# Performance work log

Hardware: AMD Instinct MI355X
Metric: run time of the kernel (lower is better)

The kernel has to match this reference:

```python
import jax, jax.numpy as jnp
import numpy as np

EPS = 1e-12  # torch F.normalize eps

def _l2n(x, axis):
    n = jnp.linalg.norm(x, axis=axis, keepdims=True)
    return x / jnp.maximum(n, EPS)

def setup_inputs() -> dict:
    key = jax.random.key(0)
    ks = jax.random.split(key, 11)
    B, N, D = 8, 4096, 512
    s = 1.0 / np.sqrt(D)
    return {
        'a': jax.random.normal(ks[0], (B, N, D), jnp.float32),
        'b': jax.random.normal(ks[1], (B, N, D), jnp.float32),
        'Wq': jax.random.normal(ks[2], (D, D), jnp.float32) * s,
        'bq': jax.random.normal(ks[3], (D,), jnp.float32) * s,
        'Wk': jax.random.normal(ks[4], (D, D), jnp.float32) * s,
        'bk': jax.random.normal(ks[5], (D,), jnp.float32) * s,
        'w_g': jax.random.normal(ks[6], (D, 1), jnp.float32),
        'Wp': jax.random.normal(ks[7], (D, D), jnp.float32) * s,
        'bp': jax.random.normal(ks[8], (D,), jnp.float32) * s,
        'Wf': jax.random.normal(ks[9], (D, D), jnp.float32) * s,
        'bf': jax.random.normal(ks[10], (D,), jnp.float32) * s,
    }

def reference(a, b, Wq, bq, Wk, bk, w_g, Wp, bp, Wf, bf):
    D = a.shape[-1]
    scale = D ** (-0.5)
    query = _l2n(jnp.einsum('bnd,ed->bne', a, Wq) + bq, axis=-1)   # [B,N,D]
    key = _l2n(jnp.einsum('bnd,ed->bne', b, Wk) + bk, axis=-1)     # [B,N,D]
    A = (query @ w_g) * scale                                      # [B,N,1]
    A = _l2n(A, axis=1)                                            # normalize over seq
    G = jnp.sum(A * query, axis=1)                                 # [B,D] learned pooling
    gk = G[:, None, :] * key                                       # broadcast [B,N,D]
    out = jnp.einsum('bnd,ed->bne', gk, Wp) + bp + query           # residual
    out = jnp.einsum('bnd,ed->bne', out, Wf) + bf
    return out
```

## Files before the change

### kernel.cpp

```cpp
#include <hip/hip_runtime.h>
#include <stdint.h>

#define DD 512
#define MTOT 32768

typedef float f32x4 __attribute__((ext_vector_type(4)));
typedef __bf16 bf16x8 __attribute__((ext_vector_type(8)));

static __device__ __forceinline__ unsigned short f2bf(float f) {
  union { float f; unsigned int u; } c; c.f = f;
  unsigned int r = c.u + 0x7fffu + ((c.u >> 16) & 1u);
  return (unsigned short)(r >> 16);
}
static __device__ __forceinline__ float bf2f(unsigned short h) {
  union { unsigned int u; float f; } c; c.u = ((unsigned int)h) << 16;
  return c.f;
}

union FragU { uint4 u; bf16x8 b; };

static __device__ __forceinline__ void load_lds16(const void* g, void* l) {
  __builtin_amdgcn_global_load_lds(
      (const __attribute__((address_space(1))) void*)g,
      (__attribute__((address_space(3))) void*)l, 16, 0, 0);
}

__global__ __launch_bounds__(256) void cvt_k(const float* __restrict__ src,
                                             unsigned short* __restrict__ dst) {
  int i = (blockIdx.x * 256 + threadIdx.x) * 4;
  float4 f = *(const float4*)(src + i);
  ushort4 h;
  h.x = f2bf(f.x); h.y = f2bf(f.y); h.z = f2bf(f.z); h.w = f2bf(f.w);
  *(ushort4*)(dst + i) = h;
}

__global__ __launch_bounds__(256) void cvt3w_k(const float* __restrict__ W0,
    const float* __restrict__ W1, const float* __restrict__ W2,
    unsigned short* __restrict__ D0, unsigned short* __restrict__ D1,
    unsigned short* __restrict__ D2) {
  int slab = blockIdx.x >> 8;
  int off = ((blockIdx.x & 255) * 256 + threadIdx.x) * 4;
  const float* s = slab == 0 ? W0 : slab == 1 ? W1 : W2;
  unsigned short* d = slab == 0 ? D0 : slab == 1 ? D1 : D2;
  float4 f = *(const float4*)(s + off);
  ushort4 h;
  h.x = f2bf(f.x); h.y = f2bf(f.y); h.z = f2bf(f.z); h.w = f2bf(f.w);
  *(ushort4*)(d + off) = h;
}

__global__ __launch_bounds__(256) void scalew_k(const float* __restrict__ Wp,
    const float* __restrict__ G, unsigned short* __restrict__ out) {
  int i = (blockIdx.x * 256 + threadIdx.x) * 4;
  int b = i >> 18;
  int rem = i & 262143;
  int d = rem & 511;
  float4 w = *(const float4*)(Wp + rem);
  float4 g = *(const float4*)(G + b * DD + d);
  ushort4 h;
  h.x = f2bf(w.x * g.x); h.y = f2bf(w.y * g.y);
  h.z = f2bf(w.z * g.z); h.w = f2bf(w.w * g.w);
  *(ushort4*)(out + i) = h;
}

template<int BBATCH, int EMODE>
__global__ __launch_bounds__(256) void gemm_k(
    const unsigned short* __restrict__ X,
    const unsigned short* __restrict__ Wb,
    const float* __restrict__ bias,
    const unsigned short* __restrict__ Qadd,
    void* __restrict__ Cv) {
  __shared__ unsigned short As[128 * 64];
  __shared__ unsigned short Bs[128 * 64];
  const int tid = threadIdx.x;
  const int lane = tid & 63, wave = tid >> 6;
  const int row0 = blockIdx.x * 128, col0 = blockIdx.y * 128;
  const unsigned short* W = Wb + (BBATCH ? (size_t)(row0 >> 12) * 262144 : 0);

  const int sr = lane >> 3;
  const int scol = ((lane & 7) ^ sr) * 8;
  const unsigned short* Ag = X + (size_t)(row0 + wave * 32 + sr) * DD + scol;
  const unsigned short* Bg = W + (size_t)(col0 + wave * 32 + sr) * DD + scol;
  const int ldsb = wave * 32 * 64;

  const int fr = lane & 15, quad = lane >> 4;
  const int wr = (wave >> 1) * 64, wc = (wave & 1) * 64;
  const int sw0 = ((quad ^ (fr & 7)) * 8);
  const int sw1 = (((quad + 4) ^ (fr & 7)) * 8);

  f32x4 acc[4][4] = {};

  for (int k0 = 0; k0 < DD; k0 += 64) {
#pragma unroll
    for (int q = 0; q < 4; q++) {
      load_lds16(Ag + (size_t)q * 8 * DD + k0, As + ldsb + q * 8 * 64);
      load_lds16(Bg + (size_t)q * 8 * DD + k0, Bs + ldsb + q * 8 * 64);
    }
    __syncthreads();
#pragma unroll
    for (int kk = 0; kk < 2; kk++) {
      const int sw = kk ? sw1 : sw0;
      bf16x8 af[4], bfr[4];
#pragma unroll
      for (int i = 0; i < 4; i++) {
        FragU u; u.u = *(const uint4*)&As[(wr + i * 16 + fr) * 64 + sw];
        af[i] = u.b;
      }
#pragma unroll
      for (int j = 0; j < 4; j++) {
        FragU u; u.u = *(const uint4*)&Bs[(wc + j * 16 + fr) * 64 + sw];
        bfr[j] = u.b;
      }
#pragma unroll
      for (int i = 0; i < 4; i++)
#pragma unroll
        for (int j = 0; j < 4; j++)
          acc[i][j] = __builtin_amdgcn_mfma_f32_16x16x32_bf16(af[i], bfr[j], acc[i][j], 0, 0, 0);
    }
    __syncthreads();
  }
#pragma unroll
  for (int j = 0; j < 4; j++) {
    int gc = col0 + wc + j * 16 + fr;
    float bv = bias[gc];
#pragma unroll
    for (int i = 0; i < 4; i++) {
      int gr0 = row0 + wr + i * 16 + quad * 4;
#pragma unroll
      for (int r = 0; r < 4; r++) {
        size_t idx = (size_t)(gr0 + r) * DD + gc;
        float v = acc[i][j][r] + bv;
        if (EMODE == 1) v += bf2f(Qadd[idx]);
        if (EMODE <= 1) ((unsigned short*)Cv)[idx] = f2bf(v);
        else            ((float*)Cv)[idx] = v;
      }
    }
  }
}

__global__ __launch_bounds__(256) void norm_k(unsigned short* __restrict__ Q,
    unsigned short* __restrict__ K, const float* __restrict__ wg,
    float* __restrict__ Araw) {
  const int lane = threadIdx.x & 63, wave = threadIdx.x >> 6;
  const size_t row = (size_t)blockIdx.x * 4 + wave;
  unsigned short* p = (blockIdx.y == 0 ? Q : K) + row * DD + lane * 8;
  uint4 u = *(uint4*)p;
  unsigned short* hp = (unsigned short*)&u;
  float v[8];
  float ss = 0.f;
#pragma unroll
  for (int t = 0; t < 8; t++) { v[t] = bf2f(hp[t]); ss += v[t] * v[t]; }
#pragma unroll
  for (int m = 1; m < 64; m <<= 1) ss += __shfl_xor(ss, m, 64);
  float inv = 1.0f / fmaxf(sqrtf(ss), 1e-12f);
#pragma unroll
  for (int t = 0; t < 8; t++) { v[t] *= inv; hp[t] = f2bf(v[t]); }
  *(uint4*)p = u;
  if (blockIdx.y == 0) {
    const float4* wp = (const float4*)(wg + lane * 8);
    float4 w0 = wp[0], w1 = wp[1];
    float dot = v[0] * w0.x + v[1] * w0.y + v[2] * w0.z + v[3] * w0.w +
                v[4] * w1.x + v[5] * w1.y + v[6] * w1.z + v[7] * w1.w;
#pragma unroll
    for (int m = 1; m < 64; m <<= 1) dot += __shfl_xor(dot, m, 64);
    if (lane == 0) Araw[row] = dot;
  }
}

__global__ __launch_bounds__(512) void reduce_s_k(const float* __restrict__ Araw,
    float* __restrict__ sinv, float* __restrict__ G) {
  const int b = blockIdx.x, t = threadIdx.x;
  G[b * DD + t] = 0.f;
  float ss = 0.f;
  for (int i = t; i < 4096; i += 512) { float v = Araw[b * 4096 + i]; ss += v * v; }
#pragma unroll
  for (int m = 1; m < 64; m <<= 1) ss += __shfl_xor(ss, m, 64);
  __shared__ float sred[8];
  if ((t & 63) == 0) sred[t >> 6] = ss;
  __syncthreads();
  if (t == 0) {
    float tot = 0.f;
    for (int i = 0; i < 8; i++) tot += sred[i];
    sinv[b] = 1.0f / fmaxf(sqrtf(tot), 1e-12f);
  }
}

__global__ __launch_bounds__(256) void pool_k(const float* __restrict__ Araw,
    const float* __restrict__ sinv, const unsigned short* __restrict__ Q,
    float* __restrict__ G) {
  const int b = blockIdx.x >> 5;
  const int chunk = blockIdx.x & 31;
  const int rbase = b * 4096 + chunk * 128;
  const float si = sinv[b];
  const int t = threadIdx.x;
  float a0 = 0.f, a1 = 0.f;
  for (int r = 0; r < 128; r++) {
    float w = Araw[rbase + r] * si;
    const unsigned short* qr = Q + (size_t)(rbase + r) * DD;
    a0 += w * bf2f(qr[t]);
    a1 += w * bf2f(qr[t + 256]);
  }
  atomicAdd(&G[b * DD + t], a0);
  atomicAdd(&G[b * DD + t + 256], a1);
}

extern "C" void kernel_launch(void* const* d_in, const int* in_sizes, int n_in,
                              void* d_out, int out_size, void* d_ws, size_t ws_size,
                              hipStream_t stream) {
  const float* a   = (const float*)d_in[0];
  const float* b   = (const float*)d_in[1];
  const float* Wq  = (const float*)d_in[2];
  const float* bq  = (const float*)d_in[3];
  const float* Wk  = (const float*)d_in[4];
  const float* bk  = (const float*)d_in[5];
  const float* wg  = (const float*)d_in[6];
  const float* Wp  = (const float*)d_in[7];
  const float* bp  = (const float*)d_in[8];
  const float* Wf  = (const float*)d_in[9];
  const float* bfb = (const float*)d_in[10];

  const size_t WELEM = 262144;
  const size_t MD = (size_t)MTOT * DD;

  unsigned short* ABb = (unsigned short*)d_ws;
  unsigned short* Qb  = ABb + MD;
  unsigned short* Kb  = Qb + MD;
  unsigned short* Wqb = Kb + MD;
  unsigned short* Wkb = Wqb + WELEM;
  unsigned short* Wfb = Wkb + WELEM;
  unsigned short* Wps = Wfb + WELEM;
  float* Araw = (float*)(Wps + 8 * WELEM);
  float* sinv = Araw + MTOT;
  float* G    = sinv + 64;

  cvt_k<<<dim3(16384), dim3(256), 0, stream>>>(a, ABb);
  cvt3w_k<<<dim3(768), dim3(256), 0, stream>>>(Wq, Wk, Wf, Wqb, Wkb, Wfb);
  gemm_k<0, 0><<<dim3(256, 4), dim3(256), 0, stream>>>(ABb, Wqb, bq, nullptr, Qb);
  cvt_k<<<dim3(16384), dim3(256), 0, stream>>>(b, ABb);
  gemm_k<0, 0><<<dim3(256, 4), dim3(256), 0, stream>>>(ABb, Wkb, bk, nullptr, Kb);
  norm_k<<<dim3(MTOT / 4, 2), dim3(256), 0, stream>>>(Qb, Kb, wg, Araw);
  reduce_s_k<<<dim3(8), dim3(512), 0, stream>>>(Araw, sinv, G);
  pool_k<<<dim3(256), dim3(256), 0, stream>>>(Araw, sinv, Qb, G);
  scalew_k<<<dim3(2048), dim3(256), 0, stream>>>(Wp, G, Wps);
  gemm_k<1, 1><<<dim3(256, 4), dim3(256), 0, stream>>>(Kb, Wps, bp, Qb, ABb);
  gemm_k<0, 2><<<dim3(256, 4), dim3(256), 0, stream>>>(ABb, Wfb, bfb, nullptr, d_out);
}
```

Baseline: 329.2 us.

## Fuse fp32->bf16 input conversion and row-norm statistics into GEMM epilogues

The Q and K projection GEMMs now read fp32 activations directly and convert them to bf16 while staging into LDS, which removes the separate conversion passes. Their epilogues accumulate per-row sums of squares and the w_g dot product through atomics. The separate normalization pass is dropped: Q and K stay unnormalized, and the per-row inverse norms are applied inside the later residual GEMM epilogue and in the pooling weights. The trade-offs are synchronous register-path loads for A in place of async LDS loads, extra atomics, and an unnormalized bf16 Q/K that changes rounding.

```diff
diff --git a/kernel.cpp b/kernel.cpp
--- a/kernel.cpp
+++ b/kernel.cpp
@@ -25,20 +25,16 @@
       (__attribute__((address_space(3))) void*)l, 16, 0, 0);
 }
 
-__global__ __launch_bounds__(256) void cvt_k(const float* __restrict__ src,
-                                             unsigned short* __restrict__ dst) {
-  int i = (blockIdx.x * 256 + threadIdx.x) * 4;
-  float4 f = *(const float4*)(src + i);
-  ushort4 h;
-  h.x = f2bf(f.x); h.y = f2bf(f.y); h.z = f2bf(f.z); h.w = f2bf(f.w);
-  *(ushort4*)(dst + i) = h;
-}
-
 __global__ __launch_bounds__(256) void cvt3w_k(const float* __restrict__ W0,
     const float* __restrict__ W1, const float* __restrict__ W2,
     unsigned short* __restrict__ D0, unsigned short* __restrict__ D1,
-    unsigned short* __restrict__ D2) {
+    unsigned short* __restrict__ D2, float* __restrict__ stats) {
   int slab = blockIdx.x >> 8;
+  if (slab == 3) {
+    int i = ((blockIdx.x - 768) * 256 + threadIdx.x) * 4;
+    *(float4*)(stats + i) = make_float4(0.f, 0.f, 0.f, 0.f);
+    return;
+  }
   int off = ((blockIdx.x & 255) * 256 + threadIdx.x) * 4;
   const float* s = slab == 0 ? W0 : slab == 1 ? W1 : W2;
   unsigned short* d = slab == 0 ? D0 : slab == 1 ? D1 : D2;
@@ -62,12 +58,17 @@
   *(ushort4*)(out + i) = h;
 }
 
-template<int BBATCH, int EMODE>
+template<int XFP32, int BBATCH, int EMODE>
 __global__ __launch_bounds__(256) void gemm_k(
-    const unsigned short* __restrict__ X,
+    const void* __restrict__ Xv,
     const unsigned short* __restrict__ Wb,
     const float* __restrict__ bias,
     const unsigned short* __restrict__ Qadd,
+    const float* __restrict__ wg,
+    float* __restrict__ ssq,
+    float* __restrict__ Pdot,
+    const float* __restrict__ qinv,
+    const float* __restrict__ kinv,
     void* __restrict__ Cv) {
   __shared__ unsigned short As[128 * 64];
   __shared__ unsigned short Bs[128 * 64];
@@ -77,10 +78,13 @@
   const unsigned short* W = Wb + (BBATCH ? (size_t)(row0 >> 12) * 262144 : 0);
 
   const int sr = lane >> 3;
-  const int scol = ((lane & 7) ^ sr) * 8;
-  const unsigned short* Ag = X + (size_t)(row0 + wave * 32 + sr) * DD + scol;
-  const unsigned short* Bg = W + (size_t)(col0 + wave * 32 + sr) * DD + scol;
+  const int c8 = lane & 7;
+  const unsigned short* Ag =
+      (const unsigned short*)Xv + (size_t)(row0 + wave * 32 + sr) * DD + (c8 ^ sr) * 8;
+  const unsigned short* Bg = W + (size_t)(col0 + wave * 32 + sr) * DD + (c8 ^ sr) * 8;
+  const float* Agf = (const float*)Xv + (size_t)(row0 + wave * 32 + sr) * DD + c8 * 8;
   const int ldsb = wave * 32 * 64;
+  const int awr = ldsb + sr * 64 + (c8 ^ sr) * 8;
 
   const int fr = lane & 15, quad = lane >> 4;
   const int wr = (wave >> 1) * 64, wc = (wave & 1) * 64;
@@ -92,7 +96,19 @@
   for (int k0 = 0; k0 < DD; k0 += 64) {
 #pragma unroll
     for (int q = 0; q < 4; q++) {
-      load_lds16(Ag + (size_t)q * 8 * DD + k0, As + ldsb + q * 8 * 64);
+      if (XFP32) {
+        const float* s = Agf + (size_t)q * 8 * DD + k0;
+        f32x4 f0 = *(const f32x4*)s;
+        f32x4 f1 = *(const f32x4*)(s + 4);
+        union { uint4 u; unsigned short h[8]; } pk;
+        pk.h[0] = f2bf(f0.x); pk.h[1] = f2bf(f0.y);
+        pk.h[2] = f2bf(f0.z); pk.h[3] = f2bf(f0.w);
+        pk.h[4] = f2bf(f1.x); pk.h[5] = f2bf(f1.y);
+        pk.h[6] = f2bf(f1.z); pk.h[7] = f2bf(f1.w);
+        *(uint4*)&As[awr + q * 8 * 64] = pk.u;
+      } else {
+        load_lds16(Ag + (size_t)q * 8 * DD + k0, As + ldsb + q * 8 * 64);
+      }
       load_lds16(Bg + (size_t)q * 8 * DD + k0, Bs + ldsb + q * 8 * 64);
     }
     __syncthreads();
@@ -118,60 +134,67 @@
     }
     __syncthreads();
   }
-#pragma unroll
-  for (int j = 0; j < 4; j++) {
-    int gc = col0 + wc + j * 16 + fr;
-    float bv = bias[gc];
-#pragma unroll
-    for (int i = 0; i < 4; i++) {
-      int gr0 = row0 + wr + i * 16 + quad * 4;
-#pragma unroll
-      for (int r = 0; r < 4; r++) {
-        size_t idx = (size_t)(gr0 + r) * DD + gc;
-        float v = acc[i][j][r] + bv;
-        if (EMODE == 1) v += bf2f(Qadd[idx]);
-        if (EMODE <= 1) ((unsigned short*)Cv)[idx] = f2bf(v);
+
+  const int colbase = col0 + wc + fr;
+  float bv4[4];
+#pragma unroll
+  for (int j = 0; j < 4; j++) bv4[j] = bias[colbase + j * 16];
+  float wg4[4];
+  if (EMODE == 1) {
+#pragma unroll
+    for (int j = 0; j < 4; j++) wg4[j] = wg[colbase + j * 16];
+  }
+#pragma unroll
+  for (int i = 0; i < 4; i++) {
+#pragma unroll
+    for (int r = 0; r < 4; r++) {
+      const int row = row0 + wr + i * 16 + quad * 4 + r;
+      float ki = 1.f, qi = 1.f;
+      if (EMODE == 3) { ki = kinv[row]; qi = qinv[row]; }
+      float ssum = 0.f, dsum = 0.f;
+#pragma unroll
+      for (int j = 0; j < 4; j++) {
+        size_t idx = (size_t)row * DD + colbase + j * 16;
+        float v;
+        if (EMODE == 3) v = acc[i][j][r] * ki + bv4[j] + qi * bf2f(Qadd[idx]);
+        else            v = acc[i][j][r] + bv4[j];
+        if (EMODE != 4) ((unsigned short*)Cv)[idx] = f2bf(v);
         else            ((float*)Cv)[idx] = v;
+        if (EMODE == 1 || EMODE == 2) ssum += v * v;
+        if (EMODE == 1) dsum += v * wg4[j];
+      }
+      if (EMODE == 1 || EMODE == 2) {
+#pragma unroll
+        for (int m = 1; m < 16; m <<= 1) ssum += __shfl_xor(ssum, m, 64);
+        if (EMODE == 1) {
+#pragma unroll
+          for (int m = 1; m < 16; m <<= 1) dsum += __shfl_xor(dsum, m, 64);
+        }
+        if (fr == 0) {
+          atomicAdd(&ssq[row], ssum);
+          if (EMODE == 1) atomicAdd(&Pdot[row], dsum);
+        }
       }
     }
   }
 }
 
-__global__ __launch_bounds__(256) void norm_k(unsigned short* __restrict__ Q,
-    unsigned short* __restrict__ K, const float* __restrict__ wg,
-    float* __restrict__ Araw) {
-  const int lane = threadIdx.x & 63, wave = threadIdx.x >> 6;
-  const size_t row = (size_t)blockIdx.x * 4 + wave;
-  unsigned short* p = (blockIdx.y == 0 ? Q : K) + row * DD + lane * 8;
-  uint4 u = *(uint4*)p;
-  unsigned short* hp = (unsigned short*)&u;
-  float v[8];
-  float ss = 0.f;
-#pragma unroll
-  for (int t = 0; t < 8; t++) { v[t] = bf2f(hp[t]); ss += v[t] * v[t]; }
-#pragma unroll
-  for (int m = 1; m < 64; m <<= 1) ss += __shfl_xor(ss, m, 64);
-  float inv = 1.0f / fmaxf(sqrtf(ss), 1e-12f);
-#pragma unroll
-  for (int t = 0; t < 8; t++) { v[t] *= inv; hp[t] = f2bf(v[t]); }
-  *(uint4*)p = u;
-  if (blockIdx.y == 0) {
-    const float4* wp = (const float4*)(wg + lane * 8);
-    float4 w0 = wp[0], w1 = wp[1];
-    float dot = v[0] * w0.x + v[1] * w0.y + v[2] * w0.z + v[3] * w0.w +
-                v[4] * w1.x + v[5] * w1.y + v[6] * w1.z + v[7] * w1.w;
-#pragma unroll
-    for (int m = 1; m < 64; m <<= 1) dot += __shfl_xor(dot, m, 64);
-    if (lane == 0) Araw[row] = dot;
-  }
-}
-
-__global__ __launch_bounds__(512) void reduce_s_k(const float* __restrict__ Araw,
-    float* __restrict__ sinv, float* __restrict__ G) {
+__global__ __launch_bounds__(512) void finstat_k(const float* __restrict__ ssqQ,
+    const float* __restrict__ ssqK, const float* __restrict__ P,
+    float* __restrict__ qinv, float* __restrict__ kinv,
+    float* __restrict__ Araw2, float* __restrict__ sinv, float* __restrict__ G) {
   const int b = blockIdx.x, t = threadIdx.x;
   G[b * DD + t] = 0.f;
   float ss = 0.f;
-  for (int i = t; i < 4096; i += 512) { float v = Araw[b * 4096 + i]; ss += v * v; }
+  for (int i = t; i < 4096; i += 512) {
+    int n = b * 4096 + i;
+    float qi = 1.0f / fmaxf(sqrtf(ssqQ[n]), 1e-12f);
+    float ki = 1.0f / fmaxf(sqrtf(ssqK[n]), 1e-12f);
+    qinv[n] = qi; kinv[n] = ki;
+    float A = P[n] * qi;
+    Araw2[n] = A * qi;
+    ss += A * A;
+  }
 #pragma unroll
   for (int m = 1; m < 64; m <<= 1) ss += __shfl_xor(ss, m, 64);
   __shared__ float sred[8];
@@ -184,7 +207,7 @@
   }
 }
 
-__global__ __launch_bounds__(256) void pool_k(const float* __restrict__ Araw,
+__global__ __launch_bounds__(256) void pool_k(const float* __restrict__ Araw2,
     const float* __restrict__ sinv, const unsigned short* __restrict__ Q,
     float* __restrict__ G) {
   const int b = blockIdx.x >> 5;
@@ -194,7 +217,7 @@
   const int t = threadIdx.x;
   float a0 = 0.f, a1 = 0.f;
   for (int r = 0; r < 128; r++) {
-    float w = Araw[rbase + r] * si;
+    float w = Araw2[rbase + r] * si;
     const unsigned short* qr = Q + (size_t)(rbase + r) * DD;
     a0 += w * bf2f(qr[t]);
     a1 += w * bf2f(qr[t + 256]);
@@ -221,26 +244,33 @@
   const size_t WELEM = 262144;
   const size_t MD = (size_t)MTOT * DD;
 
-  unsigned short* ABb = (unsigned short*)d_ws;
-  unsigned short* Qb  = ABb + MD;
+  unsigned short* O1b = (unsigned short*)d_ws;
+  unsigned short* Qb  = O1b + MD;
   unsigned short* Kb  = Qb + MD;
   unsigned short* Wqb = Kb + MD;
   unsigned short* Wkb = Wqb + WELEM;
   unsigned short* Wfb = Wkb + WELEM;
   unsigned short* Wps = Wfb + WELEM;
-  float* Araw = (float*)(Wps + 8 * WELEM);
-  float* sinv = Araw + MTOT;
-  float* G    = sinv + 64;
-
-  cvt_k<<<dim3(16384), dim3(256), 0, stream>>>(a, ABb);
-  cvt3w_k<<<dim3(768), dim3(256), 0, stream>>>(Wq, Wk, Wf, Wqb, Wkb, Wfb);
-  gemm_k<0, 0><<<dim3(256, 4), dim3(256), 0, stream>>>(ABb, Wqb, bq, nullptr, Qb);
-  cvt_k<<<dim3(16384), dim3(256), 0, stream>>>(b, ABb);
-  gemm_k<0, 0><<<dim3(256, 4), dim3(256), 0, stream>>>(ABb, Wkb, bk, nullptr, Kb);
-  norm_k<<<dim3(MTOT / 4, 2), dim3(256), 0, stream>>>(Qb, Kb, wg, Araw);
-  reduce_s_k<<<dim3(8), dim3(512), 0, stream>>>(Araw, sinv, G);
-  pool_k<<<dim3(256), dim3(256), 0, stream>>>(Araw, sinv, Qb, G);
+  float* stats = (float*)(Wps + 8 * WELEM);
+  float* ssqQ  = stats;
+  float* ssqK  = stats + MTOT;
+  float* Pd    = stats + 2 * MTOT;
+  float* qinv  = stats + 3 * MTOT;
+  float* kinv  = stats + 4 * MTOT;
+  float* Araw2 = stats + 5 * MTOT;
+  float* sinv  = stats + 6 * MTOT;
+  float* G     = sinv + 64;
+
+  cvt3w_k<<<dim3(864), dim3(256), 0, stream>>>(Wq, Wk, Wf, Wqb, Wkb, Wfb, stats);
+  gemm_k<1, 0, 1><<<dim3(256, 4), dim3(256), 0, stream>>>(
+      a, Wqb, bq, nullptr, wg, ssqQ, Pd, nullptr, nullptr, Qb);
+  gemm_k<1, 0, 2><<<dim3(256, 4), dim3(256), 0, stream>>>(
+      b, Wkb, bk, nullptr, nullptr, ssqK, nullptr, nullptr, nullptr, Kb);
+  finstat_k<<<dim3(8), dim3(512), 0, stream>>>(ssqQ, ssqK, Pd, qinv, kinv, Araw2, sinv, G);
+  pool_k<<<dim3(256), dim3(256), 0, stream>>>(Araw2, sinv, Qb, G);
   scalew_k<<<dim3(2048), dim3(256), 0, stream>>>(Wp, G, Wps);
-  gemm_k<1, 1><<<dim3(256, 4), dim3(256), 0, stream>>>(Kb, Wps, bp, Qb, ABb);
-  gemm_k<0, 2><<<dim3(256, 4), dim3(256), 0, stream>>>(ABb, Wfb, bfb, nullptr, d_out);
-}
+  gemm_k<0, 1, 3><<<dim3(256, 4), dim3(256), 0, stream>>>(
+      Kb, Wps, bp, Qb, nullptr, nullptr, nullptr, qinv, kinv, O1b);
+  gemm_k<0, 0, 4><<<dim3(256, 4), dim3(256), 0, stream>>>(
+      O1b, Wfb, bfb, nullptr, nullptr, nullptr, nullptr, nullptr, nullptr, d_out);
+}
```

New measurement: 314.8 us. -4.4%, faster.
